# Performance work log

Hardware: AMD Instinct MI355X
Metric: run time of the kernel (lower is better)

## Reference

```python
import jax, jax.numpy as jnp
import numpy as np

N = 100000        # num_nodes
F_IN = 512        # node_features
F_OUT = 2         # GCNConv out channels (hardcoded in module)
E = 3200000       # num edges (avg degree 32)


def setup_inputs() -> dict:
    key = jax.random.key(0)
    k = jax.random.split(key, 8)
    x = jax.random.normal(k[0], (N, F_IN), dtype=jnp.float32)
    edge_list = jax.random.randint(k[1], (2, E), 0, N, dtype=jnp.int64)
    edge_attr = jax.random.uniform(k[2], (E,), dtype=jnp.float32)
    # GCNConv params (glorot-ish scale)
    W = jax.random.normal(k[3], (F_IN, F_OUT), dtype=jnp.float32) / np.sqrt(F_IN)
    b = jnp.zeros((F_OUT,), dtype=jnp.float32)
    # fc head: Linear(num_nodes*2, 1)
    fc_w = jax.random.normal(k[4], (N * F_OUT,), dtype=jnp.float32) / np.sqrt(N * F_OUT)
    fc_b = jnp.zeros((), dtype=jnp.float32)
    return {"x": x, "edge_list": edge_list, "edge_attr": edge_attr,
            "W": W, "b": b, "fc_w": fc_w, "fc_b": fc_b}


def reference(x, edge_list, edge_attr, W, b, fc_w, fc_b):
    n = x.shape[0]
    row, col = edge_list[0], edge_list[1]
    # --- gcn_norm with add_self_loops=True (fill weight 1.0) ---
    loop = jnp.arange(n, dtype=edge_list.dtype)
    row_f = jnp.concatenate([row, loop])
    col_f = jnp.concatenate([col, loop])
    w_f = jnp.concatenate([edge_attr, jnp.ones((n,), dtype=edge_attr.dtype)])
    deg = jax.ops.segment_sum(w_f, col_f, num_segments=n)          # [N]
    deg_inv_sqrt = jnp.where(deg > 0, jax.lax.rsqrt(jnp.maximum(deg, 1e-30)), 0.0)
    norm = deg_inv_sqrt[row_f] * w_f * deg_inv_sqrt[col_f]          # [E+N]
    # --- linear transform then propagate (source row -> target col) ---
    h = x @ W                                                       # [N, 2]
    msg = h[row_f] * norm[:, None]                                  # [E+N, 2]
    out = jax.ops.segment_sum(msg, col_f, num_segments=n) + b      # [N, 2]
    # --- head: relu, (no dropout/noise: training=False), flatten, fc, sigmoid ---
    out = jax.nn.relu(out).reshape(-1)                              # [2N]
    logit = jnp.dot(out, fc_w) + fc_b
    return jax.nn.sigmoid(logit)
```

## Files before the change

### kernel.cpp

```cpp
#include <hip/hip_runtime.h>
#include <math.h>

#define N_NODES 100000
#define F_IN    512
#define E_EDGES 3200000

#define NR     16
#define RN     6250
#define SB     512
#define SCHUNK (E_EDGES / SB)
#define CAP    204800
#define SLICES 32
#define JMASK  0x1FFF

__global__ void k_init(int* __restrict__ cursor, float* __restrict__ logit) {
    int t = threadIdx.x;
    if (t < NR) cursor[t] = t * CAP;
    if (t == 0) logit[0] = 0.0f;
}

__global__ __launch_bounds__(256) void k_bucket(const int* __restrict__ row,
                                                const int* __restrict__ col,
                                                const float* __restrict__ w,
                                                int* __restrict__ cursor,
                                                unsigned* __restrict__ sidx,
                                                float* __restrict__ sw) {
    __shared__ int hcnt[NR];
    __shared__ int hbase[NR];
    int t = threadIdx.x;
    if (t < NR) hcnt[t] = 0;
    __syncthreads();
    int base = blockIdx.x * SCHUNK;
    for (int i = t; i < SCHUNK; i += 256) {
        int r = col[base + i] / RN;
        atomicAdd(&hcnt[r], 1);
    }
    __syncthreads();
    if (t < NR) {
        hbase[t] = atomicAdd(&cursor[t], hcnt[t]);
        hcnt[t] = 0;
    }
    __syncthreads();
    for (int i = t; i < SCHUNK; i += 256) {
        int c = col[base + i];
        int r = c / RN;
        int j = c - r * RN;
        int rank = atomicAdd(&hcnt[r], 1);
        int slot = hbase[r] + rank;
        sidx[slot] = (unsigned)j | ((unsigned)row[base + i] << 13);
        sw[slot]   = w[base + i];
    }
}

__global__ __launch_bounds__(1024) void k_deg_s(const unsigned* __restrict__ sidx,
                                                const float* __restrict__ sw,
                                                const int* __restrict__ cursor,
                                                float* __restrict__ rep_deg) {
    __shared__ float sdeg[RN];
    int r = blockIdx.x / SLICES, s = blockIdx.x % SLICES;
    int lo_r = r * CAP, hi_r = cursor[r];
    int len = hi_r - lo_r;
    int lo = lo_r + len * s / SLICES;
    int hi = lo_r + len * (s + 1) / SLICES;
    for (int j = threadIdx.x; j < RN; j += 1024) sdeg[j] = 0.0f;
    __syncthreads();
    for (int i = lo + threadIdx.x; i < hi; i += 1024) {
        unsigned u = sidx[i];
        atomicAdd(&sdeg[u & JMASK], sw[i]);
    }
    __syncthreads();
    float* out = rep_deg + (size_t)blockIdx.x * RN;
    for (int j = threadIdx.x; j < RN; j += 1024) out[j] = sdeg[j];
}

__global__ void k_dis(const float* __restrict__ rep_deg,
                      float* __restrict__ dis) {
    int i = blockIdx.x * blockDim.x + threadIdx.x;
    if (i < N_NODES) {
        int r = i / RN, j = i - r * RN;
        const float* base = rep_deg + (size_t)(r * SLICES) * RN + j;
        float d = 1.0f;
#pragma unroll
        for (int p = 0; p < SLICES; ++p) d += base[p * RN];
        dis[i] = rsqrtf(d);
    }
}

__global__ __launch_bounds__(256) void k_gemv(const float* __restrict__ x,
                                              const float* __restrict__ W,
                                              const float* __restrict__ dis,
                                              float* __restrict__ g) {
    int row  = (blockIdx.x * blockDim.x + threadIdx.x) >> 6;
    int lane = threadIdx.x & 63;
    if (row >= N_NODES) return;
    const float* xr = x + (size_t)row * F_IN;
    float a0 = 0.0f, a1 = 0.0f;
#pragma unroll
    for (int c = 0; c < 2; ++c) {
        int k = c * 256 + lane * 4;
        float4 xv  = *(const float4*)(xr + k);
        float4 w01 = *(const float4*)(W + 2 * k);
        float4 w23 = *(const float4*)(W + 2 * k + 4);
        a0 += xv.x * w01.x + xv.y * w01.z + xv.z * w23.x + xv.w * w23.z;
        a1 += xv.x * w01.y + xv.y * w01.w + xv.z * w23.y + xv.w * w23.w;
    }
#pragma unroll
    for (int off = 32; off > 0; off >>= 1) {
        a0 += __shfl_down(a0, off, 64);
        a1 += __shfl_down(a1, off, 64);
    }
    if (lane == 0) {
        float d = dis[row];
        g[2 * row]     = a0 * d;
        g[2 * row + 1] = a1 * d;
    }
}

__global__ __launch_bounds__(1024) void k_prop_s(const unsigned* __restrict__ sidx,
                                                 const float* __restrict__ sw,
                                                 const int* __restrict__ cursor,
                                                 const float* __restrict__ g,
                                                 float* __restrict__ rep_acc) {
    __shared__ float sacc[RN * 2];
    int r = blockIdx.x / SLICES, s = blockIdx.x % SLICES;
    int lo_r = r * CAP, hi_r = cursor[r];
    int len = hi_r - lo_r;
    int lo = lo_r + len * s / SLICES;
    int hi = lo_r + len * (s + 1) / SLICES;
    for (int j = threadIdx.x; j < RN * 2; j += 1024) sacc[j] = 0.0f;
    __syncthreads();
    for (int i = lo + threadIdx.x; i < hi; i += 1024) {
        unsigned u = sidx[i];
        int j  = u & JMASK;
        int rr = u >> 13;
        float we = sw[i];
        float2 gv = *(const float2*)(g + 2 * rr);
        atomicAdd(&sacc[2 * j],     gv.x * we);
        atomicAdd(&sacc[2 * j + 1], gv.y * we);
    }
    __syncthreads();
    float* out = rep_acc + (size_t)blockIdx.x * (RN * 2);
    for (int j = threadIdx.x; j < RN * 2; j += 1024) out[j] = sacc[j];
}

__global__ __launch_bounds__(256) void k_epilogue(const float* __restrict__ rep_acc,
                                                  const float* __restrict__ g,
                                                  const float* __restrict__ dis,
                                                  const float* __restrict__ b,
                                                  const float* __restrict__ fc_w,
                                                  float* __restrict__ logit) {
    int i = blockIdx.x * blockDim.x + threadIdx.x;
    float partial = 0.0f;
    if (i < N_NODES) {
        int r = i / RN, j = i - r * RN;
        const float2* base = (const float2*)rep_acc + (size_t)(r * SLICES) * RN + j;
        float o0 = 0.0f, o1 = 0.0f;
#pragma unroll
        for (int p = 0; p < SLICES; ++p) { float2 v = base[p * RN]; o0 += v.x; o1 += v.y; }
        float d = dis[i];
        o0 = (o0 + g[2 * i])     * d + b[0];
        o1 = (o1 + g[2 * i + 1]) * d + b[1];
        o0 = fmaxf(o0, 0.0f); o1 = fmaxf(o1, 0.0f);
        partial = o0 * fc_w[2 * i] + o1 * fc_w[2 * i + 1];
    }
#pragma unroll
    for (int off = 32; off > 0; off >>= 1)
        partial += __shfl_down(partial, off, 64);
    __shared__ float sdata[4];
    int lane = threadIdx.x & 63, wid = threadIdx.x >> 6;
    if (lane == 0) sdata[wid] = partial;
    __syncthreads();
    if (threadIdx.x == 0)
        atomicAdd(logit, sdata[0] + sdata[1] + sdata[2] + sdata[3]);
}

__global__ void k_sigmoid(const float* __restrict__ logit,
                          const float* __restrict__ fc_b,
                          float* __restrict__ out) {
    float z = logit[0] + fc_b[0];
    out[0] = 1.0f / (1.0f + expf(-z));
}


__global__ void k_init_f(float* __restrict__ deg, float* __restrict__ accum,
                         float* __restrict__ logit) {
    int i = blockIdx.x * blockDim.x + threadIdx.x;
    if (i < N_NODES) {
        deg[i] = 1.0f;
        accum[2 * i] = 0.0f;
        accum[2 * i + 1] = 0.0f;
    }
    if (i == 0) logit[0] = 0.0f;
}

__global__ void k_deg_f(const int* __restrict__ col, const float* __restrict__ w,
                        float* __restrict__ deg) {
    int e = blockIdx.x * blockDim.x + threadIdx.x;
    if (e < E_EDGES) atomicAdd(&deg[col[e]], w[e]);
}

__global__ void k_rsqrt_f(float* __restrict__ deg) {
    int i = blockIdx.x * blockDim.x + threadIdx.x;
    if (i < N_NODES) deg[i] = rsqrtf(deg[i]);
}

__global__ void k_prop_f(const int* __restrict__ row, const int* __restrict__ col,
                         const float* __restrict__ w, const float* __restrict__ dis,
                         const float* __restrict__ g, float* __restrict__ accum) {
    int e = blockIdx.x * blockDim.x + threadIdx.x;
    if (e < E_EDGES) {
        int r = row[e], c = col[e];
        float nm = w[e];
        atomicAdd(&accum[2 * c],     g[2 * r] * nm);
        atomicAdd(&accum[2 * c + 1], g[2 * r + 1] * nm);
    }
}

__global__ __launch_bounds__(256) void k_epilogue_f(const float* __restrict__ accum,
                                                    const float* __restrict__ g,
                                                    const float* __restrict__ dis,
                                                    const float* __restrict__ b,
                                                    const float* __restrict__ fc_w,
                                                    float* __restrict__ logit) {
    int i = blockIdx.x * blockDim.x + threadIdx.x;
    float partial = 0.0f;
    if (i < N_NODES) {
        float d = dis[i];
        float o0 = (accum[2 * i]     + g[2 * i])     * d + b[0];
        float o1 = (accum[2 * i + 1] + g[2 * i + 1]) * d + b[1];
        o0 = fmaxf(o0, 0.0f); o1 = fmaxf(o1, 0.0f);
        partial = o0 * fc_w[2 * i] + o1 * fc_w[2 * i + 1];
    }
#pragma unroll
    for (int off = 32; off > 0; off >>= 1)
        partial += __shfl_down(partial, off, 64);
    __shared__ float sdata[4];
    int lane = threadIdx.x & 63, wid = threadIdx.x >> 6;
    if (lane == 0) sdata[wid] = partial;
    __syncthreads();
    if (threadIdx.x == 0)
        atomicAdd(logit, sdata[0] + sdata[1] + sdata[2] + sdata[3]);
}


extern "C" void kernel_launch(void* const* d_in, const int* in_sizes, int n_in,
                              void* d_out, int out_size, void* d_ws, size_t ws_size,
                              hipStream_t stream) {
    const float* x   = (const float*)d_in[0];
    const int*   el  = (const int*)d_in[1];
    const float* ea  = (const float*)d_in[2];
    const float* W   = (const float*)d_in[3];
    const float* b   = (const float*)d_in[4];
    const float* fcw = (const float*)d_in[5];
    const float* fcb = (const float*)d_in[6];
    float*       out = (float*)d_out;

    const int* row = el;
    const int* col = el + E_EDGES;

    float* ws = (float*)d_ws;
    const int TB = 256;
    dim3 gN((N_NODES + TB - 1) / TB);
    dim3 gG((N_NODES * 64 + TB - 1) / TB);

    size_t o_g    = 0;
    size_t o_dis  = o_g + 2 * N_NODES;
    size_t o_log  = o_dis + N_NODES;
    size_t o_cur  = (o_log + 64) & ~63ull;
    size_t o_sidx = (o_cur + 64) & ~63ull;
    size_t o_sw   = o_sidx + (size_t)NR * CAP;
    size_t o_rd   = o_sw + (size_t)NR * CAP;
    size_t o_ra   = o_rd + (size_t)NR * SLICES * RN;
    size_t need_fast = (o_ra + (size_t)NR * SLICES * RN * 2) * 4;

    if (ws_size >= need_fast) {
        float*    g       = ws + o_g;
        float*    dis     = ws + o_dis;
        float*    logit   = ws + o_log;
        int*      cursor  = (int*)(ws + o_cur);
        unsigned* sidx    = (unsigned*)(ws + o_sidx);
        float*    sw      = ws + o_sw;
        float*    rep_deg = ws + o_rd;
        float*    rep_acc = ws + o_ra;

        k_init    <<<1, 64, 0, stream>>>(cursor, logit);
        k_bucket  <<<SB, 256, 0, stream>>>(row, col, ea, cursor, sidx, sw);
        k_deg_s   <<<NR * SLICES, 1024, 0, stream>>>(sidx, sw, cursor, rep_deg);
        k_dis     <<<gN, TB, 0, stream>>>(rep_deg, dis);
        k_gemv    <<<gG, TB, 0, stream>>>(x, W, dis, g);
        k_prop_s  <<<NR * SLICES, 1024, 0, stream>>>(sidx, sw, cursor, g, rep_acc);
        k_epilogue<<<gN, TB, 0, stream>>>(rep_acc, g, dis, b, fcw, logit);
        k_sigmoid <<<1, 1, 0, stream>>>(logit, fcb, out);
    } else {
        float* deg   = ws;
        float* g     = ws + N_NODES;
        float* accum = ws + 3 * N_NODES;
        float* logit = ws + 5 * N_NODES;
        dim3 gE((E_EDGES + TB - 1) / TB);
        k_init_f    <<<gN, TB, 0, stream>>>(deg, accum, logit);
        k_deg_f     <<<gE, TB, 0, stream>>>(col, ea, deg);
        k_rsqrt_f   <<<gN, TB, 0, stream>>>(deg);
        k_gemv      <<<gG, TB, 0, stream>>>(x, W, deg, g);
        k_prop_f    <<<gE, TB, 0, stream>>>(row, col, ea, deg, g, accum);
        k_epilogue_f<<<gN, TB, 0, stream>>>(accum, g, deg, b, fcw, logit);
        k_sigmoid   <<<1, 1, 0, stream>>>(logit, fcb, out);
    }
}
```

Measured before the change: 415.1 us.

## Pack edge records into 64-bit words, fuse degree reduction and sigmoid, retune buckets

Edge index and weight are packed into a single 64-bit record, so the bucket, degree and propagation passes read one stream instead of two. The degree-slice reduction and rsqrt move into the gemv kernel, which uses a wave shuffle over the slices. The final sigmoid is folded into the epilogue through a last-block ticket counter. Bucket geometry changes to 32 buckets of 3125 nodes with 16 slices, 640 bucket blocks and vectorized int4 loads, and a memset replaces the init kernel. Together these cut launches and memory traffic. The costs are wider per-edge records and a 12-bit local index that must hold up to 3124, which leaves the source row only 20 bits (100000 fits).

```diff
diff --git a/kernel.cpp b/kernel.cpp
--- a/kernel.cpp
+++ b/kernel.cpp
@@ -5,95 +5,97 @@
 #define F_IN    512
 #define E_EDGES 3200000
 
-#define NR     16
-#define RN     6250
-#define SB     512
+#define NR     32
+#define RN     3125
+#define SB     640
 #define SCHUNK (E_EDGES / SB)
-#define CAP    204800
-#define SLICES 32
-#define JMASK  0x1FFF
-
-__global__ void k_init(int* __restrict__ cursor, float* __restrict__ logit) {
-    int t = threadIdx.x;
-    if (t < NR) cursor[t] = t * CAP;
-    if (t == 0) logit[0] = 0.0f;
-}
+#define CAP    102400
+#define SLICES 16
+#define JBITS  12
+#define JMASK  0xFFF
+
+#define C_LOGIT 32
+#define C_DONE  33
 
 __global__ __launch_bounds__(256) void k_bucket(const int* __restrict__ row,
                                                 const int* __restrict__ col,
                                                 const float* __restrict__ w,
-                                                int* __restrict__ cursor,
-                                                unsigned* __restrict__ sidx,
-                                                float* __restrict__ sw) {
+                                                int* __restrict__ ctrl,
+                                                unsigned long long* __restrict__ rec) {
     __shared__ int hcnt[NR];
     __shared__ int hbase[NR];
     int t = threadIdx.x;
     if (t < NR) hcnt[t] = 0;
     __syncthreads();
     int base = blockIdx.x * SCHUNK;
-    for (int i = t; i < SCHUNK; i += 256) {
-        int r = col[base + i] / RN;
-        atomicAdd(&hcnt[r], 1);
+    const int* colc = col + base;
+    for (int i4 = t * 4; i4 < SCHUNK; i4 += 1024) {
+        int4 c4 = *(const int4*)(colc + i4);
+        atomicAdd(&hcnt[c4.x / RN], 1);
+        atomicAdd(&hcnt[c4.y / RN], 1);
+        atomicAdd(&hcnt[c4.z / RN], 1);
+        atomicAdd(&hcnt[c4.w / RN], 1);
     }
     __syncthreads();
     if (t < NR) {
-        hbase[t] = atomicAdd(&cursor[t], hcnt[t]);
+        hbase[t] = atomicAdd(&ctrl[t], hcnt[t]);
         hcnt[t] = 0;
     }
     __syncthreads();
-    for (int i = t; i < SCHUNK; i += 256) {
-        int c = col[base + i];
-        int r = c / RN;
-        int j = c - r * RN;
-        int rank = atomicAdd(&hcnt[r], 1);
-        int slot = hbase[r] + rank;
-        sidx[slot] = (unsigned)j | ((unsigned)row[base + i] << 13);
-        sw[slot]   = w[base + i];
-    }
-}
-
-__global__ __launch_bounds__(1024) void k_deg_s(const unsigned* __restrict__ sidx,
-                                                const float* __restrict__ sw,
-                                                const int* __restrict__ cursor,
+    const int* rowc = row + base;
+    const float* wc = w + base;
+    for (int i4 = t * 4; i4 < SCHUNK; i4 += 1024) {
+        int4   c4 = *(const int4*)(colc + i4);
+        int4   r4 = *(const int4*)(rowc + i4);
+        float4 w4 = *(const float4*)(wc + i4);
+#pragma unroll
+        for (int q = 0; q < 4; ++q) {
+            int c = (&c4.x)[q];
+            int r = c / RN;
+            int j = c - r * RN;
+            int rank = atomicAdd(&hcnt[r], 1);
+            int slot = r * CAP + hbase[r] + rank;
+            unsigned idx = (unsigned)j | ((unsigned)(&r4.x)[q] << JBITS);
+            rec[slot] = ((unsigned long long)__float_as_uint((&w4.x)[q]) << 32) | idx;
+        }
+    }
+}
+
+__global__ __launch_bounds__(1024) void k_deg_s(const unsigned long long* __restrict__ rec,
+                                                const int* __restrict__ ctrl,
                                                 float* __restrict__ rep_deg) {
     __shared__ float sdeg[RN];
     int r = blockIdx.x / SLICES, s = blockIdx.x % SLICES;
-    int lo_r = r * CAP, hi_r = cursor[r];
-    int len = hi_r - lo_r;
-    int lo = lo_r + len * s / SLICES;
-    int hi = lo_r + len * (s + 1) / SLICES;
+    int len = ctrl[r];
+    int lo = r * CAP + len * s / SLICES;
+    int hi = r * CAP + len * (s + 1) / SLICES;
     for (int j = threadIdx.x; j < RN; j += 1024) sdeg[j] = 0.0f;
     __syncthreads();
     for (int i = lo + threadIdx.x; i < hi; i += 1024) {
-        unsigned u = sidx[i];
-        atomicAdd(&sdeg[u & JMASK], sw[i]);
+        unsigned long long u = rec[i];
+        atomicAdd(&sdeg[(unsigned)u & JMASK], __uint_as_float((unsigned)(u >> 32)));
     }
     __syncthreads();
     float* out = rep_deg + (size_t)blockIdx.x * RN;
     for (int j = threadIdx.x; j < RN; j += 1024) out[j] = sdeg[j];
 }
 
-__global__ void k_dis(const float* __restrict__ rep_deg,
-                      float* __restrict__ dis) {
-    int i = blockIdx.x * blockDim.x + threadIdx.x;
-    if (i < N_NODES) {
-        int r = i / RN, j = i - r * RN;
-        const float* base = rep_deg + (size_t)(r * SLICES) * RN + j;
-        float d = 1.0f;
-#pragma unroll
-        for (int p = 0; p < SLICES; ++p) d += base[p * RN];
-        dis[i] = rsqrtf(d);
-    }
-}
-
 __global__ __launch_bounds__(256) void k_gemv(const float* __restrict__ x,
                                               const float* __restrict__ W,
-                                              const float* __restrict__ dis,
+                                              const float* __restrict__ rep_deg,
+                                              float* __restrict__ dis,
                                               float* __restrict__ g) {
-    int row  = (blockIdx.x * blockDim.x + threadIdx.x) >> 6;
+    int rowi = (blockIdx.x * blockDim.x + threadIdx.x) >> 6;
     int lane = threadIdx.x & 63;
-    if (row >= N_NODES) return;
-    const float* xr = x + (size_t)row * F_IN;
+    if (rowi >= N_NODES) return;
+    int rr = rowi / RN, j = rowi - rr * RN;
+    float dv = 0.0f;
+    if (lane < SLICES) dv = rep_deg[(size_t)(rr * SLICES + lane) * RN + j];
+    dv += __shfl_xor(dv, 1, 64);
+    dv += __shfl_xor(dv, 2, 64);
+    dv += __shfl_xor(dv, 4, 64);
+    dv += __shfl_xor(dv, 8, 64);
+    const float* xr = x + (size_t)rowi * F_IN;
     float a0 = 0.0f, a1 = 0.0f;
 #pragma unroll
     for (int c = 0; c < 2; ++c) {
@@ -110,30 +112,30 @@
         a1 += __shfl_down(a1, off, 64);
     }
     if (lane == 0) {
-        float d = dis[row];
-        g[2 * row]     = a0 * d;
-        g[2 * row + 1] = a1 * d;
-    }
-}
-
-__global__ __launch_bounds__(1024) void k_prop_s(const unsigned* __restrict__ sidx,
-                                                 const float* __restrict__ sw,
-                                                 const int* __restrict__ cursor,
+        float d = rsqrtf(1.0f + dv);
+        dis[rowi] = d;
+        g[2 * rowi]     = a0 * d;
+        g[2 * rowi + 1] = a1 * d;
+    }
+}
+
+__global__ __launch_bounds__(1024) void k_prop_s(const unsigned long long* __restrict__ rec,
+                                                 const int* __restrict__ ctrl,
                                                  const float* __restrict__ g,
                                                  float* __restrict__ rep_acc) {
     __shared__ float sacc[RN * 2];
     int r = blockIdx.x / SLICES, s = blockIdx.x % SLICES;
-    int lo_r = r * CAP, hi_r = cursor[r];
-    int len = hi_r - lo_r;
-    int lo = lo_r + len * s / SLICES;
-    int hi = lo_r + len * (s + 1) / SLICES;
+    int len = ctrl[r];
+    int lo = r * CAP + len * s / SLICES;
+    int hi = r * CAP + len * (s + 1) / SLICES;
     for (int j = threadIdx.x; j < RN * 2; j += 1024) sacc[j] = 0.0f;
     __syncthreads();
     for (int i = lo + threadIdx.x; i < hi; i += 1024) {
-        unsigned u = sidx[i];
-        int j  = u & JMASK;
-        int rr = u >> 13;
-        float we = sw[i];
+        unsigned long long u = rec[i];
+        unsigned idx = (unsigned)u;
+        int j  = idx & JMASK;
+        int rr = idx >> JBITS;
+        float we = __uint_as_float((unsigned)(u >> 32));
         float2 gv = *(const float2*)(g + 2 * rr);
         atomicAdd(&sacc[2 * j],     gv.x * we);
         atomicAdd(&sacc[2 * j + 1], gv.y * we);
@@ -148,7 +150,10 @@
                                                   const float* __restrict__ dis,
                                                   const float* __restrict__ b,
                                                   const float* __restrict__ fc_w,
-                                                  float* __restrict__ logit) {
+                                                  const float* __restrict__ fc_b,
+                                                  int* __restrict__ ctrl,
+                                                  float* __restrict__ out) {
+    float* logit = (float*)&ctrl[C_LOGIT];
     int i = blockIdx.x * blockDim.x + threadIdx.x;
     float partial = 0.0f;
     if (i < N_NODES) {
@@ -170,15 +175,15 @@
     int lane = threadIdx.x & 63, wid = threadIdx.x >> 6;
     if (lane == 0) sdata[wid] = partial;
     __syncthreads();
-    if (threadIdx.x == 0)
+    if (threadIdx.x == 0) {
         atomicAdd(logit, sdata[0] + sdata[1] + sdata[2] + sdata[3]);
-}
-
-__global__ void k_sigmoid(const float* __restrict__ logit,
-                          const float* __restrict__ fc_b,
-                          float* __restrict__ out) {
-    float z = logit[0] + fc_b[0];
-    out[0] = 1.0f / (1.0f + expf(-z));
+        __threadfence();
+        int ticket = atomicAdd(&ctrl[C_DONE], 1);
+        if (ticket == (int)gridDim.x - 1) {
+            float z = atomicAdd(logit, 0.0f) + fc_b[0];
+            out[0] = 1.0f / (1.0f + expf(-z));
+        }
+    }
 }
 
 
@@ -204,15 +209,44 @@
     if (i < N_NODES) deg[i] = rsqrtf(deg[i]);
 }
 
+__global__ __launch_bounds__(256) void k_gemv_f(const float* __restrict__ x,
+                                                const float* __restrict__ W,
+                                                const float* __restrict__ dis,
+                                                float* __restrict__ g) {
+    int rowi = (blockIdx.x * blockDim.x + threadIdx.x) >> 6;
+    int lane = threadIdx.x & 63;
+    if (rowi >= N_NODES) return;
+    const float* xr = x + (size_t)rowi * F_IN;
+    float a0 = 0.0f, a1 = 0.0f;
+#pragma unroll
+    for (int c = 0; c < 2; ++c) {
+        int k = c * 256 + lane * 4;
+        float4 xv  = *(const float4*)(xr + k);
+        float4 w01 = *(const float4*)(W + 2 * k);
+        float4 w23 = *(const float4*)(W + 2 * k + 4);
+        a0 += xv.x * w01.x + xv.y * w01.z + xv.z * w23.x + xv.w * w23.z;
+        a1 += xv.x * w01.y + xv.y * w01.w + xv.z * w23.y + xv.w * w23.w;
+    }
+#pragma unroll
+    for (int off = 32; off > 0; off >>= 1) {
+        a0 += __shfl_down(a0, off, 64);
+        a1 += __shfl_down(a1, off, 64);
+    }
+    if (lane == 0) {
+        float d = dis[rowi];
+        g[2 * rowi] = a0 * d;
+        g[2 * rowi + 1] = a1 * d;
+    }
+}
+
 __global__ void k_prop_f(const int* __restrict__ row, const int* __restrict__ col,
-                         const float* __restrict__ w, const float* __restrict__ dis,
-                         const float* __restrict__ g, float* __restrict__ accum) {
+                         const float* __restrict__ w, const float* __restrict__ g,
+                         float* __restrict__ accum) {
     int e = blockIdx.x * blockDim.x + threadIdx.x;
     if (e < E_EDGES) {
         int r = row[e], c = col[e];
-        float nm = w[e];
-        atomicAdd(&accum[2 * c],     g[2 * r] * nm);
-        atomicAdd(&accum[2 * c + 1], g[2 * r + 1] * nm);
+        atomicAdd(&accum[2 * c],     g[2 * r] * w[e]);
+        atomicAdd(&accum[2 * c + 1], g[2 * r + 1] * w[e]);
     }
 }
 
@@ -242,6 +276,13 @@
         atomicAdd(logit, sdata[0] + sdata[1] + sdata[2] + sdata[3]);
 }
 
+__global__ void k_sigmoid_f(const float* __restrict__ logit,
+                            const float* __restrict__ fc_b,
+                            float* __restrict__ out) {
+    float z = logit[0] + fc_b[0];
+    out[0] = 1.0f / (1.0f + expf(-z));
+}
+
 
 extern "C" void kernel_launch(void* const* d_in, const int* in_sizes, int n_in,
                               void* d_out, int out_size, void* d_ws, size_t ws_size,
@@ -263,34 +304,28 @@
     dim3 gN((N_NODES + TB - 1) / TB);
     dim3 gG((N_NODES * 64 + TB - 1) / TB);
 
-    size_t o_g    = 0;
+    size_t o_ctrl = 0;
+    size_t o_g    = 64;
     size_t o_dis  = o_g + 2 * N_NODES;
-    size_t o_log  = o_dis + N_NODES;
-    size_t o_cur  = (o_log + 64) & ~63ull;
-    size_t o_sidx = (o_cur + 64) & ~63ull;
-    size_t o_sw   = o_sidx + (size_t)NR * CAP;
-    size_t o_rd   = o_sw + (size_t)NR * CAP;
+    size_t o_rec  = (o_dis + N_NODES + 63) & ~63ull;
+    size_t o_rd   = o_rec + (size_t)NR * CAP * 2;
     size_t o_ra   = o_rd + (size_t)NR * SLICES * RN;
     size_t need_fast = (o_ra + (size_t)NR * SLICES * RN * 2) * 4;
 
     if (ws_size >= need_fast) {
-        float*    g       = ws + o_g;
-        float*    dis     = ws + o_dis;
-        float*    logit   = ws + o_log;
-        int*      cursor  = (int*)(ws + o_cur);
-        unsigned* sidx    = (unsigned*)(ws + o_sidx);
-        float*    sw      = ws + o_sw;
-        float*    rep_deg = ws + o_rd;
-        float*    rep_acc = ws + o_ra;
-
-        k_init    <<<1, 64, 0, stream>>>(cursor, logit);
-        k_bucket  <<<SB, 256, 0, stream>>>(row, col, ea, cursor, sidx, sw);
-        k_deg_s   <<<NR * SLICES, 1024, 0, stream>>>(sidx, sw, cursor, rep_deg);
-        k_dis     <<<gN, TB, 0, stream>>>(rep_deg, dis);
-        k_gemv    <<<gG, TB, 0, stream>>>(x, W, dis, g);
-        k_prop_s  <<<NR * SLICES, 1024, 0, stream>>>(sidx, sw, cursor, g, rep_acc);
-        k_epilogue<<<gN, TB, 0, stream>>>(rep_acc, g, dis, b, fcw, logit);
-        k_sigmoid <<<1, 1, 0, stream>>>(logit, fcb, out);
+        int*                ctrl    = (int*)(ws + o_ctrl);
+        float*              g       = ws + o_g;
+        float*              dis     = ws + o_dis;
+        unsigned long long* rec     = (unsigned long long*)(ws + o_rec);
+        float*              rep_deg = ws + o_rd;
+        float*              rep_acc = ws + o_ra;
+
+        hipMemsetAsync(ctrl, 0, 64 * sizeof(int), stream);
+        k_bucket  <<<SB, 256, 0, stream>>>(row, col, ea, ctrl, rec);
+        k_deg_s   <<<NR * SLICES, 1024, 0, stream>>>(rec, ctrl, rep_deg);
+        k_gemv    <<<gG, TB, 0, stream>>>(x, W, rep_deg, dis, g);
+        k_prop_s  <<<NR * SLICES, 1024, 0, stream>>>(rec, ctrl, g, rep_acc);
+        k_epilogue<<<gN, TB, 0, stream>>>(rep_acc, g, dis, b, fcw, fcb, ctrl, out);
     } else {
         float* deg   = ws;
         float* g     = ws + N_NODES;
@@ -300,9 +335,9 @@
         k_init_f    <<<gN, TB, 0, stream>>>(deg, accum, logit);
         k_deg_f     <<<gE, TB, 0, stream>>>(col, ea, deg);
         k_rsqrt_f   <<<gN, TB, 0, stream>>>(deg);
-        k_gemv      <<<gG, TB, 0, stream>>>(x, W, deg, g);
-        k_prop_f    <<<gE, TB, 0, stream>>>(row, col, ea, deg, g, accum);
+        k_gemv_f    <<<gG, TB, 0, stream>>>(x, W, deg, g);
+        k_prop_f    <<<gE, TB, 0, stream>>>(row, col, ea, g, accum);
         k_epilogue_f<<<gN, TB, 0, stream>>>(accum, g, deg, b, fcw, logit);
-        k_sigmoid   <<<1, 1, 0, stream>>>(logit, fcb, out);
-    }
-}
+        k_sigmoid_f <<<1, 1, 0, stream>>>(logit, fcb, out);
+    }
+}
```

Result: faster. 400.8 us (-3.4%).
